# Kernel tuning notes

Measured on AMD Instinct MI355X. Metric: run time of the kernel, lower is better.

## Reference

```python
import jax, jax.numpy as jnp
import numpy as np

T, N = 20, 32768          # seq_length, numNodes
D_IN, D_EMB, D_H, D_OUT = 2, 64, 128, 5


def setup_inputs() -> dict:
    key = jax.random.key(0)
    ks = jax.random.split(key, 12)
    s = 0.05
    return {
        "nodes": jax.random.normal(ks[0], (T, N, D_IN), jnp.float32),
        "present_mask": jax.random.randint(ks[1], (T, N), 0, 2).astype(bool),
        "hidden_states": jax.random.normal(ks[2], (N, D_H), jnp.float32),
        "cell_states": jax.random.normal(ks[3], (N, D_H), jnp.float32),
        "W_embed": jax.random.normal(ks[4], (D_IN, D_EMB), jnp.float32) * s,
        "b_embed": jnp.zeros((D_EMB,), jnp.float32),
        "W_ih": jax.random.normal(ks[5], (D_EMB, 4 * D_H), jnp.float32) * s,
        "b_ih": jnp.zeros((4 * D_H,), jnp.float32),
        "W_hh": jax.random.normal(ks[6], (D_H, 4 * D_H), jnp.float32) * s,
        "b_hh": jnp.zeros((4 * D_H,), jnp.float32),
        "W_out": jax.random.normal(ks[7], (D_H, D_OUT), jnp.float32) * s,
        "b_out": jnp.zeros((D_OUT,), jnp.float32),
    }


def reference(nodes, present_mask, hidden_states, cell_states,
              W_embed, b_embed, W_ih, b_ih, W_hh, b_hh, W_out, b_out):
    # Per-frame: gather present nodes -> embed+ReLU (dropout=eval identity)
    # -> LSTMCell -> scatter h/c/output back. Gather+scatter is expressed as
    # a masked update, which is mathematically identical.
    def step(carry, frame):
        h, c = carry
        x, mask = frame                      # x: [N,2], mask: [N]
        emb = jax.nn.relu(x @ W_embed + b_embed)              # [N,Demb]
        gates = emb @ W_ih + b_ih + h @ W_hh + b_hh           # [N,4H]
        i, f, g, o = jnp.split(gates, 4, axis=-1)             # torch order
        i, f, o = jax.nn.sigmoid(i), jax.nn.sigmoid(f), jax.nn.sigmoid(o)
        g = jnp.tanh(g)
        c_new = f * c + i * g
        h_new = o * jnp.tanh(c_new)
        m = mask[:, None]
        h = jnp.where(m, h_new, h)
        c = jnp.where(m, c_new, c)
        out = jnp.where(m, h_new @ W_out + b_out, 0.0)        # absent -> zeros
        return (h, c), out

    (h_fin, c_fin), outputs = jax.lax.scan(
        step, (hidden_states, cell_states), (nodes, present_mask))
    return outputs, h_fin, c_fin                              # [T,N,5],[N,H],[N,H]
```

## Files before the change

### kernel.cpp

```cpp
#include <hip/hip_runtime.h>
#include <cstddef>


typedef __attribute__((ext_vector_type(8))) short  s16x8;
typedef __attribute__((ext_vector_type(4))) float  f32x4;

namespace {
constexpr int T_STEPS = 20;
constexpr int NN      = 32768;
constexpr int D_EMB   = 64;
constexpr int D_H     = 128;
constexpr int D_OUT   = 5;
constexpr int G4      = 512;
constexpr int MT      = 64;
constexpr int BLOCK   = 512;
constexpr int GRID    = NN / MT;
constexpr int WP_ELEMS   = 8 * 4 * 6 * 64 * 8;
constexpr int WOUT_ELEMS = 4 * 64 * 8;
constexpr int A_ELEMS    = 24 * 64 * 8;
constexpr float LOG2E = 1.4426950408889634f;
constexpr size_t OFF_H = (size_t)T_STEPS * NN * D_OUT;
constexpr size_t OFF_C = OFF_H + (size_t)NN * D_H;
}

__device__ __forceinline__ unsigned short f2bf(float x) {
    unsigned u = __float_as_uint(x);
    u = (u + 0x7FFFu + ((u >> 16) & 1u)) >> 16;
    return (unsigned short)u;
}
__device__ __forceinline__ unsigned short f2bf_hw(float x) {
    __bf16 b = (__bf16)x;
    union { __bf16 b; unsigned short u; } cv;
    cv.b = b;
    return cv.u;
}
__device__ __forceinline__ float bf2f(unsigned short h) {
    return __uint_as_float(((unsigned)h) << 16);
}
__device__ __forceinline__ float exp2f_fast(float x) {
#if __has_builtin(__builtin_amdgcn_exp2f)
    return __builtin_amdgcn_exp2f(x);
#else
    return __expf(x * 0.6931471805599453f);
#endif
}
__device__ __forceinline__ float sig_pre(float a) {
    return __builtin_amdgcn_rcpf(1.0f + exp2f_fast(a));
}

__global__ void prepack_kernel(const float* __restrict__ W_ih,
                               const float* __restrict__ b_ih,
                               const float* __restrict__ W_hh,
                               const float* __restrict__ b_hh,
                               const float* __restrict__ W_out,
                               unsigned short* __restrict__ Wp,
                               unsigned short* __restrict__ WoutF,
                               float* __restrict__ b_sum) {
    int idx = blockIdx.x * blockDim.x + threadIdx.x;
    if (idx < WP_ELEMS) {
        int j    = idx & 7;
        int L    = (idx >> 3) & 63;
        int rest = idx >> 9;
        int kb   = rest % 6;
        int gw   = rest / 6;
        int g    = gw & 3, w = gw >> 2;
        int k    = kb * 32 + (L >> 4) * 8 + j;
        int col  = g * D_H + w * 16 + (L & 15);
        float v  = (k < D_EMB) ? W_ih[k * G4 + col] : W_hh[(k - D_EMB) * G4 + col];
        float s  = (g == 2) ? (2.0f * LOG2E) : (-LOG2E);
        Wp[idx] = f2bf(v * s);
    } else if (idx < WP_ELEMS + WOUT_ELEMS) {
        int i2 = idx - WP_ELEMS;
        int j = i2 & 7, L = (i2 >> 3) & 63, kb2 = i2 >> 9;
        int k = kb2 * 32 + (L >> 4) * 8 + j;
        int n = L & 15;
        WoutF[i2] = (n < D_OUT) ? f2bf(W_out[k * D_OUT + n]) : (unsigned short)0;
    }
    if (idx < G4) {
        int g = idx / D_H;
        float s = (g == 2) ? (2.0f * LOG2E) : (-LOG2E);
        b_sum[idx] = (b_ih[idx] + b_hh[idx]) * s;
    }
}

__global__ __launch_bounds__(BLOCK, 2) void vlstm_kernel(
    const float* __restrict__ nodes,
    const int*   __restrict__ mask,
    const float* __restrict__ h0,
    const float* __restrict__ c0,
    const float* __restrict__ W_embed,
    const float* __restrict__ b_embed,
    const float* __restrict__ b_out,
    const unsigned short* __restrict__ Wp,
    const unsigned short* __restrict__ WoutF,
    const float* __restrict__ b_sum,
    float* __restrict__ out)
{
    __shared__ __align__(16) unsigned short A[2][A_ELEMS];
    __shared__ __align__(16) float st_out[2][MT * D_OUT];
    __shared__ float We_s[2 * D_EMB];
    __shared__ float be_s[D_EMB];
    __shared__ unsigned long long msk64[2];

    const int tid  = threadIdx.x;
    const int wave = tid >> 6;
    const int L    = tid & 63;
    const int quad = L >> 4;
    const int l15  = L & 15;
    const int n_base = blockIdx.x * MT;

    const unsigned short* wbase = Wp + (size_t)wave * (4 * 6 * 64 * 8);
    s16x8 Bf[4][6];
    #pragma unroll
    for (int g = 0; g < 4; g++)
        #pragma unroll
        for (int kb = 0; kb < 6; kb++)
            Bf[g][kb] = *(const s16x8*)(wbase + ((g * 6 + kb) * 64 + L) * 8);
    s16x8 WoF[4];
    #pragma unroll
    for (int kb2 = 0; kb2 < 4; kb2++)
        WoF[kb2] = *(const s16x8*)(WoutF + ((kb2 * 64) + L) * 8);

    const int u_lane = wave * 16 + l15;
    float bias[4];
    #pragma unroll
    for (int g = 0; g < 4; g++) bias[g] = b_sum[g * D_H + wave * 16 + l15];
    const float bo = (l15 < D_OUT) ? b_out[l15] : 0.0f;

    const int kb_u = 2 + (u_lane >> 5);
    const int fl   = ((u_lane >> 3) & 3) * 16 + quad * 4;
    const int j_u  = u_lane & 7;

    for (int i = tid; i < 3 * D_EMB; i += BLOCK) {
        if (i < 2 * D_EMB) We_s[i] = W_embed[i];
        else               be_s[i - 2 * D_EMB] = b_embed[i - 2 * D_EMB];
    }

    float          c2[4][4];
    unsigned short hr[4][4];
    #pragma unroll
    for (int rt = 0; rt < 4; rt++)
        #pragma unroll
        for (int r = 0; r < 4; r++) {
            int m = rt * 16 + quad * 4 + r;
            c2[rt][r] = 2.0f * c0[(size_t)(n_base + m) * D_H + u_lane];
            hr[rt][r] = f2bf_hw(h0[(size_t)(n_base + m) * D_H + u_lane]);
            A[0][((rt * 6 + kb_u) * 64 + fl + r) * 8 + j_u] = hr[rt][r];
        }

    const int node_e = tid >> 3;
    const int eb     = tid & 7;
    const int idx_e  = (((node_e >> 4) * 6 + (eb >> 2)) * 64 + (eb & 3) * 16 + (node_e & 15)) * 8;
    {
        const float2* xp = (const float2*)(nodes + ((size_t)0 * NN + n_base + node_e) * 2);
        float2 x = *xp;
        s16x8 ev;
        #pragma unroll
        for (int j = 0; j < 8; j++) {
            int e = eb * 8 + j;
            float v = fmaf(x.x, We_s[e], fmaf(x.y, We_s[D_EMB + e], be_s[e]));
            ev[j] = (short)f2bf_hw(fmaxf(v, 0.0f));
        }
        *(s16x8*)(&A[0][idx_e]) = ev;
        if (wave == 0) {
            int lm0 = mask[n_base + L];
            unsigned long long bm0 = __ballot(lm0 != 0);
            if (L == 0) msk64[0] = bm0;
        }
    }
    __syncthreads();

    for (int t = 0; t < T_STEPS; t++) {
        unsigned short* __restrict__ Ar = A[t & 1];
        unsigned short* __restrict__ Aw = A[(t + 1) & 1];

        float2 xv = make_float2(0.0f, 0.0f);
        int    lm = 0;
        if (t + 1 < T_STEPS) {
            xv = *(const float2*)(nodes + ((size_t)(t + 1) * NN + n_base + node_e) * 2);
            if (wave == 0) lm = mask[(size_t)(t + 1) * NN + n_base + L];
        }
        const unsigned long long M = msk64[t & 1];

        f32x4 acc[4][4];
        #pragma unroll
        for (int rt = 0; rt < 4; rt++)
            #pragma unroll
            for (int g = 0; g < 4; g++)
                acc[rt][g] = (f32x4){bias[g], bias[g], bias[g], bias[g]};
        #pragma unroll
        for (int kb = 0; kb < 6; kb++) {
            #pragma unroll
            for (int rt = 0; rt < 4; rt++) {
                s16x8 af = *(const s16x8*)(Ar + ((rt * 6 + kb) * 64 + L) * 8);
                #pragma unroll
                for (int g = 0; g < 4; g++)
                    acc[rt][g] = __builtin_amdgcn_mfma_f32_16x16x32_bf16(
                        af, Bf[g][kb], acc[rt][g], 0, 0, 0);
            }
        }

        #pragma unroll
        for (int rt = 0; rt < 4; rt++) {
            unsigned nib = (unsigned)(M >> (rt * 16 + quad * 4)) & 0xFu;
            #pragma unroll
            for (int r = 0; r < 4; r++) {
                float gi = sig_pre(acc[rt][0][r]);
                float gf = sig_pre(acc[rt][1][r]);
                float rg = sig_pre(acc[rt][2][r]);
                float go = sig_pre(acc[rt][3][r]);
                float gg2 = fmaf(-4.0f, rg, 2.0f);
                float cn2 = fmaf(gf, c2[rt][r], gi * gg2);
                float rr = __builtin_amdgcn_rcpf(1.0f + exp2f_fast(cn2 * LOG2E));
                float hv = go * fmaf(-2.0f, rr, 1.0f);
                unsigned short hb = f2bf_hw(hv);
                if ((nib >> r) & 1u) { c2[rt][r] = cn2; hr[rt][r] = hb; }
                Aw[((rt * 6 + kb_u) * 64 + fl + r) * 8 + j_u] = hr[rt][r];
            }
        }

        if (t + 1 < T_STEPS) {
            s16x8 ev;
            #pragma unroll
            for (int j = 0; j < 8; j++) {
                int e = eb * 8 + j;
                float v = fmaf(xv.x, We_s[e], fmaf(xv.y, We_s[D_EMB + e], be_s[e]));
                ev[j] = (short)f2bf_hw(fmaxf(v, 0.0f));
            }
            *(s16x8*)(Aw + idx_e) = ev;
            if (wave == 0) {
                unsigned long long bm = __ballot(lm != 0);
                if (L == 0) msk64[(t + 1) & 1] = bm;
            }
        }

        __syncthreads();

        if (t > 0 && wave >= 4) {
            int j = tid - 256;
            if (j < MT * D_OUT / 4)
                ((f32x4*)(out + ((size_t)(t - 1) * NN + n_base) * D_OUT))[j] =
                    ((const f32x4*)st_out[(t - 1) & 1])[j];
        }

        if (wave < 4) {
            f32x4 ao = (f32x4){0.0f, 0.0f, 0.0f, 0.0f};
            #pragma unroll
            for (int kb2 = 0; kb2 < 4; kb2++) {
                s16x8 af = *(const s16x8*)(Aw + ((wave * 6 + 2 + kb2) * 64 + L) * 8);
                ao = __builtin_amdgcn_mfma_f32_16x16x32_bf16(af, WoF[kb2], ao, 0, 0, 0);
            }
            if (l15 < D_OUT) {
                unsigned nib_o = (unsigned)(M >> (wave * 16 + quad * 4)) & 0xFu;
                #pragma unroll
                for (int r = 0; r < 4; r++) {
                    int node = wave * 16 + quad * 4 + r;
                    st_out[t & 1][node * D_OUT + l15] =
                        ((nib_o >> r) & 1u) ? (ao[r] + bo) : 0.0f;
                }
            }
        }
    }

    __syncthreads();
    if (tid < MT * D_OUT / 4)
        ((f32x4*)(out + ((size_t)(T_STEPS - 1) * NN + n_base) * D_OUT))[tid] =
            ((const f32x4*)st_out[(T_STEPS - 1) & 1])[tid];

    for (int i = tid; i < MT * D_H; i += BLOCK) {
        int node = i >> 7, u = i & 127;
        int k = D_EMB + u;
        int idx = (((node >> 4) * 6 + (k >> 5)) * 64 + ((k >> 3) & 3) * 16 + (node & 15)) * 8 + (k & 7);
        out[OFF_H + (size_t)(n_base + node) * D_H + u] = bf2f(A[0][idx]);
    }

    __syncthreads();
    float* cs = (float*)A;
    #pragma unroll
    for (int rt = 0; rt < 4; rt++)
        #pragma unroll
        for (int r = 0; r < 4; r++) {
            int m = rt * 16 + quad * 4 + r;
            cs[m * 129 + u_lane] = 0.5f * c2[rt][r];
        }
    __syncthreads();
    for (int i = tid; i < MT * D_H; i += BLOCK) {
        int node = i >> 7, u = i & 127;
        out[OFF_C + (size_t)(n_base + node) * D_H + u] = cs[node * 129 + u];
    }
}

extern "C" void kernel_launch(void* const* d_in, const int* in_sizes, int n_in,
                              void* d_out, int out_size, void* d_ws, size_t ws_size,
                              hipStream_t stream) {
    const float* nodes   = (const float*)d_in[0];
    const int*   mask    = (const int*)  d_in[1];
    const float* h0      = (const float*)d_in[2];
    const float* c0      = (const float*)d_in[3];
    const float* W_embed = (const float*)d_in[4];
    const float* b_embed = (const float*)d_in[5];
    const float* W_ih    = (const float*)d_in[6];
    const float* b_ih    = (const float*)d_in[7];
    const float* W_hh    = (const float*)d_in[8];
    const float* b_hh    = (const float*)d_in[9];
    const float* W_out   = (const float*)d_in[10];
    const float* b_out   = (const float*)d_in[11];
    float* out = (float*)d_out;

    unsigned short* Wp    = (unsigned short*)d_ws;
    unsigned short* WoutF = Wp + WP_ELEMS;
    float*          b_sum = (float*)(WoutF + WOUT_ELEMS);

    prepack_kernel<<<(WP_ELEMS + WOUT_ELEMS + 255) / 256, 256, 0, stream>>>(
        W_ih, b_ih, W_hh, b_hh, W_out, Wp, WoutF, b_sum);

    vlstm_kernel<<<GRID, BLOCK, 0, stream>>>(
        nodes, mask, h0, c0, W_embed, b_embed, b_out, Wp, WoutF, b_sum, out);
}
```

Measured before the change: 282.9 us.

## Interleave per-row-tile MFMA gate GEMMs with LSTM activations and prescale cell state

Splits the recurrent gate GEMM into per-row-tile chunks and interleaves them with the activation math for earlier tiles, so MFMA work overlaps with the transcendental and VALU work. The embedding and mask computation is placed between activation chunks. The cell state is now kept prescaled by 2*log2(e), which removes a multiply from the tanh path, and the bias is used directly as the first MFMA accumulator instead of a separate initialisation. The scheduling relies on the compiler keeping the order and may raise register pressure.

```diff
diff --git a/kernel.cpp b/kernel.cpp
--- a/kernel.cpp
+++ b/kernel.cpp
@@ -19,6 +19,9 @@
 constexpr int WOUT_ELEMS = 4 * 64 * 8;
 constexpr int A_ELEMS    = 24 * 64 * 8;
 constexpr float LOG2E = 1.4426950408889634f;
+constexpr float AM4   = -4.0f * LOG2E;
+constexpr float AP2   =  2.0f * LOG2E;
+constexpr float CINV  = 0.34657359027997264f;
 constexpr size_t OFF_H = (size_t)T_STEPS * NN * D_OUT;
 constexpr size_t OFF_C = OFF_H + (size_t)NN * D_H;
 }
@@ -122,9 +125,12 @@
         WoF[kb2] = *(const s16x8*)(WoutF + ((kb2 * 64) + L) * 8);
 
     const int u_lane = wave * 16 + l15;
-    float bias[4];
-    #pragma unroll
-    for (int g = 0; g < 4; g++) bias[g] = b_sum[g * D_H + wave * 16 + l15];
+    f32x4 biasv[4];
+    #pragma unroll
+    for (int g = 0; g < 4; g++) {
+        float b = b_sum[g * D_H + wave * 16 + l15];
+        biasv[g] = (f32x4){b, b, b, b};
+    }
     const float bo = (l15 < D_OUT) ? b_out[l15] : 0.0f;
 
     const int kb_u = 2 + (u_lane >> 5);
@@ -136,14 +142,14 @@
         else               be_s[i - 2 * D_EMB] = b_embed[i - 2 * D_EMB];
     }
 
-    float          c2[4][4];
+    float          cL[4][4];
     unsigned short hr[4][4];
     #pragma unroll
     for (int rt = 0; rt < 4; rt++)
         #pragma unroll
         for (int r = 0; r < 4; r++) {
             int m = rt * 16 + quad * 4 + r;
-            c2[rt][r] = 2.0f * c0[(size_t)(n_base + m) * D_H + u_lane];
+            cL[rt][r] = AP2 * c0[(size_t)(n_base + m) * D_H + u_lane];
             hr[rt][r] = f2bf_hw(h0[(size_t)(n_base + m) * D_H + u_lane]);
             A[0][((rt * 6 + kb_u) * 64 + fl + r) * 8 + j_u] = hr[rt][r];
         }
@@ -170,6 +176,39 @@
     }
     __syncthreads();
 
+#define GEMM_RT(rt) do {                                                       \
+    {   s16x8 af0 = *(const s16x8*)(Ar + (((rt) * 6 + 0) * 64 + L) * 8);       \
+        _Pragma("unroll")                                                      \
+        for (int g = 0; g < 4; g++)                                            \
+            acc[rt][g] = __builtin_amdgcn_mfma_f32_16x16x32_bf16(              \
+                af0, Bf[g][0], biasv[g], 0, 0, 0); }                           \
+    _Pragma("unroll")                                                          \
+    for (int kb = 1; kb < 6; kb++) {                                           \
+        s16x8 af = *(const s16x8*)(Ar + (((rt) * 6 + kb) * 64 + L) * 8);       \
+        _Pragma("unroll")                                                      \
+        for (int g = 0; g < 4; g++)                                            \
+            acc[rt][g] = __builtin_amdgcn_mfma_f32_16x16x32_bf16(              \
+                af, Bf[g][kb], acc[rt][g], 0, 0, 0); }                         \
+} while (0)
+
+#define ACT_RT(rt) do {                                                        \
+    unsigned nib = (unsigned)(M >> ((rt) * 16 + quad * 4)) & 0xFu;             \
+    _Pragma("unroll")                                                          \
+    for (int r = 0; r < 4; r++) {                                              \
+        float gi = sig_pre(acc[rt][0][r]);                                     \
+        float gf = sig_pre(acc[rt][1][r]);                                     \
+        float rg = sig_pre(acc[rt][2][r]);                                     \
+        float go = sig_pre(acc[rt][3][r]);                                     \
+        float ggL = fmaf(AM4, rg, AP2);                   \
+        float cnL = fmaf(gf, cL[rt][r], gi * ggL);        \
+        float rr  = __builtin_amdgcn_rcpf(1.0f + exp2f_fast(cnL));             \
+        float hv  = go * fmaf(-2.0f, rr, 1.0f);           \
+        unsigned short hb = f2bf_hw(hv);                                       \
+        if ((nib >> r) & 1u) { cL[rt][r] = cnL; hr[rt][r] = hb; }              \
+        Aw[(((rt) * 6 + kb_u) * 64 + fl + r) * 8 + j_u] = hr[rt][r];           \
+    }                                                                          \
+} while (0)
+
     for (int t = 0; t < T_STEPS; t++) {
         unsigned short* __restrict__ Ar = A[t & 1];
         unsigned short* __restrict__ Aw = A[(t + 1) & 1];
@@ -183,41 +222,12 @@
         const unsigned long long M = msk64[t & 1];
 
         f32x4 acc[4][4];
-        #pragma unroll
-        for (int rt = 0; rt < 4; rt++)
-            #pragma unroll
-            for (int g = 0; g < 4; g++)
-                acc[rt][g] = (f32x4){bias[g], bias[g], bias[g], bias[g]};
-        #pragma unroll
-        for (int kb = 0; kb < 6; kb++) {
-            #pragma unroll
-            for (int rt = 0; rt < 4; rt++) {
-                s16x8 af = *(const s16x8*)(Ar + ((rt * 6 + kb) * 64 + L) * 8);
-                #pragma unroll
-                for (int g = 0; g < 4; g++)
-                    acc[rt][g] = __builtin_amdgcn_mfma_f32_16x16x32_bf16(
-                        af, Bf[g][kb], acc[rt][g], 0, 0, 0);
-            }
-        }
-
-        #pragma unroll
-        for (int rt = 0; rt < 4; rt++) {
-            unsigned nib = (unsigned)(M >> (rt * 16 + quad * 4)) & 0xFu;
-            #pragma unroll
-            for (int r = 0; r < 4; r++) {
-                float gi = sig_pre(acc[rt][0][r]);
-                float gf = sig_pre(acc[rt][1][r]);
-                float rg = sig_pre(acc[rt][2][r]);
-                float go = sig_pre(acc[rt][3][r]);
-                float gg2 = fmaf(-4.0f, rg, 2.0f);
-                float cn2 = fmaf(gf, c2[rt][r], gi * gg2);
-                float rr = __builtin_amdgcn_rcpf(1.0f + exp2f_fast(cn2 * LOG2E));
-                float hv = go * fmaf(-2.0f, rr, 1.0f);
-                unsigned short hb = f2bf_hw(hv);
-                if ((nib >> r) & 1u) { c2[rt][r] = cn2; hr[rt][r] = hb; }
-                Aw[((rt * 6 + kb_u) * 64 + fl + r) * 8 + j_u] = hr[rt][r];
-            }
-        }
+        GEMM_RT(0);
+        GEMM_RT(1);
+        GEMM_RT(2);
+        ACT_RT(0);
+        GEMM_RT(3);
+        ACT_RT(1);
 
         if (t + 1 < T_STEPS) {
             s16x8 ev;
@@ -233,6 +243,9 @@
                 if (L == 0) msk64[(t + 1) & 1] = bm;
             }
         }
+
+        ACT_RT(2);
+        ACT_RT(3);
 
         __syncthreads();
 
@@ -261,6 +274,8 @@
             }
         }
     }
+#undef GEMM_RT
+#undef ACT_RT
 
     __syncthreads();
     if (tid < MT * D_OUT / 4)
@@ -281,7 +296,7 @@
         #pragma unroll
         for (int r = 0; r < 4; r++) {
             int m = rt * 16 + quad * 4 + r;
-            cs[m * 129 + u_lane] = 0.5f * c2[rt][r];
+            cs[m * 129 + u_lane] = CINV * cL[rt][r];
         }
     __syncthreads();
     for (int i = tid; i < MT * D_H; i += BLOCK) {
```

After: 274.3 us. -3.1%, faster.
